# Optimization experiments

Hardware: AMD Instinct MI355X
Metric: run time of the kernel (lower is better)

The kernel has to match this reference:

```python
import jax, jax.numpy as jnp
import numpy as np

H, D, TOPK, NUM_B = 8, 64, 32, 1000
DIM, BATCH, SEQ = 1024, 4, 2048
SCALE = D ** -0.5


def _kaiming_like(key, shape, fan_in):
    # matches init.kaiming_uniform_(a=sqrt(5)) => U(-1/sqrt(fan_in), 1/sqrt(fan_in)) scale
    bound = 1.0 / np.sqrt(fan_in)
    return jax.random.uniform(key, shape, jnp.float32, -bound, bound)


def setup_inputs() -> dict:
    key = jax.random.key(0)
    ks = jax.random.split(key, 7)
    inner = H * D
    x = jax.random.normal(ks[0], (BATCH, SEQ, DIM), jnp.float32)
    W_qv = _kaiming_like(ks[1], (DIM, 2 * inner), DIM)
    W_out = _kaiming_like(ks[2], (inner, DIM), inner)
    b_out = jnp.zeros((DIM,), jnp.float32)
    b_mat = _kaiming_like(ks[3], (NUM_B, D, D), D)
    k_vec = _kaiming_like(ks[4], (NUM_B, D), D)
    o_vec = _kaiming_like(ks[5], (NUM_B, D), D)
    return {"x": x, "W_qv": W_qv, "W_out": W_out, "b_out": b_out,
            "b_mat": b_mat, "k_vec": k_vec, "o_vec": o_vec}


def reference(x, W_qv, W_out, b_out, b_mat, k_vec, o_vec):
    B, I, _ = x.shape
    qv = x @ W_qv                                   # (B, I, 2*H*D)
    q, v = jnp.split(qv, 2, axis=-1)

    def to_bh(t):                                    # 'b i (h d) -> (b h) i d'
        return t.reshape(B, I, H, D).transpose(0, 2, 1, 3).reshape(B * H, I, D)

    q, v = to_bh(q), to_bh(v)
    sim = jnp.einsum('nd,bid->bin', k_vec, q) * SCALE        # (B*H, I, num_b)
    t, b_inds = jax.lax.top_k(sim, TOPK)                     # (B*H, I, K) each
    attn = jax.nn.softmax(t, axis=-1)
    # torch einsum 'b i k d d, b i d -> b i k d' (repeated d) == diagonal of brains
    diag_b = jnp.diagonal(b_mat, axis1=-2, axis2=-1)         # (num_b, D)
    membr_pot = diag_b[b_inds] * v[:, :, None, :]            # (B*H, I, K, D)
    spike_proba = jax.nn.sigmoid(membr_pot)
    # straight-through rounding
    spike = spike_proba + jax.lax.stop_gradient(jnp.round(spike_proba) - spike_proba)
    nrt = spike * o_vec[b_inds]                              # (B*H, I, K, D)
    # psi starts as zeros_like(o) and is scatter-written at b_inds (last-write on dups)
    psi = jnp.zeros_like(o_vec).at[b_inds].set((1.0 - spike_proba) * membr_pot)
    out = jnp.einsum('bikd,bik->bid', nrt, attn)             # (B*H, I, D)
    out = out.reshape(B, H, I, D).transpose(0, 2, 1, 3).reshape(B, I, H * D)
    return out @ W_out + b_out, psi
```

## Files before the change

### kernel.cpp

```cpp
#include <hip/hip_runtime.h>
#include <math.h>

#define H_     8
#define D_     64
#define TOPK_  32
#define NUMB_  1000
#define DIM_   1024
#define BATCH_ 4
#define SEQ_   2048
#define INNER_ 512
#define TOK_   (BATCH_*SEQ_)
#define ROWS_  (BATCH_*H_*SEQ_)

#define PH_TOK_  4096
#define PH_ROWS_ 32768


__global__ void k0_prep(const float* __restrict__ b_mat,
                        const float* __restrict__ k_vec,
                        float* __restrict__ diagD,
                        float* __restrict__ kT,
                        int*   __restrict__ psiRow) {
    int t = blockIdx.x * 256 + threadIdx.x;
    if (t < NUMB_ * D_) {
        int n = t >> 6, d = t & 63;
        diagD[t] = b_mat[n * (D_ * D_) + d * (D_ + 1)];
        kT[d * NUMB_ + n] = k_vec[t];
    }
    if (t < NUMB_) psiRow[t] = -1;
}

#define BK1 16
__global__ __launch_bounds__(256) void k1_qv(const float* __restrict__ x,
                                             const float* __restrict__ Wqv,
                                             double* __restrict__ Qh,
                                             float*  __restrict__ V,
                                             int tokBase) {
    __shared__ float xs[64][BK1 + 1];
    __shared__ float ws[BK1][64 + 1];
    const int tx = threadIdx.x & 15, ty = threadIdx.x >> 4;
    const int mBase = tokBase + blockIdx.y * 64;
    const int nBase = blockIdx.x * 64;

    double acc[4][4];
#pragma unroll
    for (int a = 0; a < 4; a++)
#pragma unroll
        for (int b = 0; b < 4; b++) acc[a][b] = 0.0;

    for (int k0 = 0; k0 < DIM_; k0 += BK1) {
        for (int i = threadIdx.x; i < 64 * BK1; i += 256) {
            int r = i >> 4, kk = i & 15;
            xs[r][kk] = x[(size_t)(mBase + r) * DIM_ + k0 + kk];
        }
        for (int i = threadIdx.x; i < BK1 * 64; i += 256) {
            int kk = i >> 6, c = i & 63;
            ws[kk][c] = Wqv[(size_t)(k0 + kk) * (2 * INNER_) + nBase + c];
        }
        __syncthreads();
#pragma unroll
        for (int kk = 0; kk < BK1; ++kk) {
            float xa[4], wb[4];
#pragma unroll
            for (int a = 0; a < 4; a++) xa[a] = xs[ty * 4 + a][kk];
#pragma unroll
            for (int b = 0; b < 4; b++) wb[b] = ws[kk][tx * 4 + b];
#pragma unroll
            for (int a = 0; a < 4; a++)
#pragma unroll
                for (int b = 0; b < 4; b++)
                    acc[a][b] += (double)xa[a] * (double)wb[b];
        }
        __syncthreads();
    }

    const int mr = mBase + ty * 4, nc = nBase + tx * 4;
    if (nc < INNER_) {
#pragma unroll
        for (int a = 0; a < 4; a++)
#pragma unroll
            for (int b = 0; b < 4; b++)
                Qh[(size_t)(mr - tokBase + a) * INNER_ + nc + b] = acc[a][b];
    } else {
#pragma unroll
        for (int a = 0; a < 4; a++)
#pragma unroll
            for (int b = 0; b < 4; b++)
                V[(size_t)(mr + a) * INNER_ + (nc - INNER_) + b] = (float)acc[a][b];
    }
}

__global__ __launch_bounds__(256) void k2_sim(const double* __restrict__ Qh,
                                              const float*  __restrict__ V,
                                              const float*  __restrict__ kT,
                                              const float*  __restrict__ diagD,
                                              const float*  __restrict__ o_vec,
                                              float* __restrict__ OutMid,
                                              int*   __restrict__ psiRow,
                                              int sBase0, int tokOff) {
    __shared__ double qld[4][4][64];
    const int lane = threadIdx.x & 63;
    const int wid  = threadIdx.x >> 6;
    const int g    = blockIdx.x * 4 + wid;
    const int sBase = sBase0 + g * 4;

#pragma unroll
    for (int r = 0; r < 4; r++) {
        int s = sBase + r;
        int b = s >> 14, h = (s >> 11) & 7, i = s & 2047;
        int tok = b * SEQ_ + i;
        qld[wid][r][lane] = Qh[(size_t)(tok - tokOff) * INNER_ + h * D_ + lane];
    }
    __syncthreads();

    double acc[4][16];
#pragma unroll
    for (int r = 0; r < 4; r++)
#pragma unroll
        for (int nb = 0; nb < 16; nb++) acc[r][nb] = 0.0;

    for (int d = 0; d < 64; ++d) {
        double q0 = qld[wid][0][d];
        double q1 = qld[wid][1][d];
        double q2 = qld[wid][2][d];
        double q3 = qld[wid][3][d];
        const float* kp = kT + d * NUMB_;
#pragma unroll
        for (int nb = 0; nb < 16; ++nb) {
            int n = nb * 64 + lane;
            float kv = (n < NUMB_) ? kp[n] : 0.f;
            double kd = (double)kv;
            acc[0][nb] += q0 * kd;
            acc[1][nb] += q1 * kd;
            acc[2][nb] += q2 * kd;
            acc[3][nb] += q3 * kd;
        }
    }

#pragma unroll
    for (int r = 0; r < 4; r++) {
        int s = sBase + r;
        int b = s >> 14, h = (s >> 11) & 7, i = s & 2047;
        int tok = b * SEQ_ + i;
        float vlane = V[(size_t)tok * INNER_ + h * D_ + lane];

        unsigned key[16];
#pragma unroll
        for (int nb = 0; nb < 16; ++nb) {
            int n = nb * 64 + lane;
            float f = (float)acc[r][nb];
            unsigned u = __float_as_uint(f);
            unsigned kk = (u & 0x80000000u) ? ~u : (u | 0x80000000u);
            key[nb] = (n < NUMB_) ? kk : 0u;
        }

        unsigned tau = 0u;
        for (int bit = 31; bit >= 0; --bit) {
            unsigned cand = tau | (1u << bit);
            int c = 0;
#pragma unroll
            for (int nb = 0; nb < 16; ++nb)
                c += __popcll(__ballot(key[nb] >= cand));
            if (c >= TOPK_) tau = cand;
        }

        float esum = 0.f, outAcc = 0.f;
        int cgt = 0;

#pragma unroll
        for (int nb = 0; nb < 16; ++nb) {
            bool isgt = (key[nb] > tau);
            unsigned long long mm = __ballot(isgt);
            cgt += __popcll(mm);
            if (isgt) atomicMax(psiRow + nb * 64 + lane, s);
            while (mm) {
                int l = __ffsll((long long)mm) - 1; mm &= mm - 1;
                int n = nb * 64 + l;
                double v = __shfl(acc[r][nb], l);
                float ek = expf((float)v * 0.125f);
                esum += ek;
                float dg = diagD[n * 64 + lane];
                float mpot = dg * vlane;
                if (mpot > 0.f) outAcc += ek * o_vec[n * 64 + lane];
            }
        }

        int needed = TOPK_ - cgt;
        int ceq = 0;
#pragma unroll
        for (int nb = 0; nb < 16; ++nb)
            ceq += __popcll(__ballot(key[nb] == tau));

        if (ceq == needed) {
#pragma unroll
            for (int nb = 0; nb < 16; ++nb) {
                bool iseq = (key[nb] == tau);
                unsigned long long mm = __ballot(iseq);
                if (iseq) atomicMax(psiRow + nb * 64 + lane, s);
                while (mm) {
                    int l = __ffsll((long long)mm) - 1; mm &= mm - 1;
                    int n = nb * 64 + l;
                    double v = __shfl(acc[r][nb], l);
                    float ek = expf((float)v * 0.125f);
                    esum += ek;
                    float dg = diagD[n * 64 + lane];
                    float mpot = dg * vlane;
                    if (mpot > 0.f) outAcc += ek * o_vec[n * 64 + lane];
                }
            }
        } else {
            unsigned takenMask = 0u;
            for (int t = 0; t < needed; ++t) {
                double bv = -1e300; int bn = 0x7fffffff;
#pragma unroll
                for (int nb = 0; nb < 16; ++nb) {
                    int n = nb * 64 + lane;
                    bool candt = (key[nb] == tau) && !(takenMask & (1u << nb))
                                 && (n < NUMB_);
                    double v = acc[r][nb];
                    if (candt && (v > bv || (v == bv && n < bn))) { bv = v; bn = n; }
                }
                for (int off = 32; off; off >>= 1) {
                    double ov = __shfl_xor(bv, off);
                    int    on = __shfl_xor(bn, off);
                    if (ov > bv || (ov == bv && on < bn)) { bv = ov; bn = on; }
                }
                if ((bn & 63) == lane) takenMask |= 1u << (bn >> 6);
                float ek = expf((float)bv * 0.125f);
                esum += ek;
                float dg = diagD[bn * 64 + lane];
                float mpot = dg * vlane;
                if (mpot > 0.f) outAcc += ek * o_vec[bn * 64 + lane];
                if (lane == 0) atomicMax(psiRow + bn, s);
            }
        }

        OutMid[(size_t)tok * INNER_ + h * D_ + lane] = outAcc / esum;
    }
}

#define BK3 16
__global__ __launch_bounds__(256) void k3_out(const float* __restrict__ A,
                                              const float* __restrict__ Wout,
                                              const float* __restrict__ bout,
                                              float* __restrict__ out) {
    __shared__ float as[64][BK3 + 1];
    __shared__ float bs[BK3][64 + 1];
    const int tx = threadIdx.x & 15, ty = threadIdx.x >> 4;
    const int mBase = blockIdx.y * 64, nBase = blockIdx.x * 64;

    float acc[4][4];
#pragma unroll
    for (int a = 0; a < 4; a++)
#pragma unroll
        for (int b = 0; b < 4; b++) acc[a][b] = 0.f;

    for (int k0 = 0; k0 < INNER_; k0 += BK3) {
        for (int i = threadIdx.x; i < 64 * BK3; i += 256) {
            int r = i >> 4, kk = i & 15;
            as[r][kk] = A[(size_t)(mBase + r) * INNER_ + k0 + kk];
        }
        for (int i = threadIdx.x; i < BK3 * 64; i += 256) {
            int kk = i >> 6, c = i & 63;
            bs[kk][c] = Wout[(size_t)(k0 + kk) * DIM_ + nBase + c];
        }
        __syncthreads();
#pragma unroll
        for (int kk = 0; kk < BK3; ++kk) {
            float xa[4], wb[4];
#pragma unroll
            for (int a = 0; a < 4; a++) xa[a] = as[ty * 4 + a][kk];
#pragma unroll
            for (int b = 0; b < 4; b++) wb[b] = bs[kk][tx * 4 + b];
#pragma unroll
            for (int a = 0; a < 4; a++)
#pragma unroll
                for (int b = 0; b < 4; b++)
                    acc[a][b] += xa[a] * wb[b];
        }
        __syncthreads();
    }

    const int mr = mBase + ty * 4, nc = nBase + tx * 4;
#pragma unroll
    for (int a = 0; a < 4; a++)
#pragma unroll
        for (int b = 0; b < 4; b++)
            out[(size_t)(mr + a) * DIM_ + nc + b] = acc[a][b] + bout[nc + b];
}

__global__ void k4_psi(const int*   __restrict__ psiRow,
                       const float* __restrict__ V,
                       const float* __restrict__ diagD,
                       float* __restrict__ psiOut) {
    int t = blockIdx.x * 256 + threadIdx.x;
    if (t >= NUMB_ * D_) return;
    int n = t >> 6, d = t & 63;
    int s = psiRow[n];
    float val = 0.f;
    if (s >= 0) {
        int b = s >> 14, h = (s >> 11) & 7, i = s & 2047;
        int tok = b * SEQ_ + i;
        float v  = V[(size_t)tok * INNER_ + h * D_ + d];
        float m  = diagD[t] * v;
        float sg = 1.f / (1.f + expf(-m));
        val = (1.f - sg) * m;
    }
    psiOut[t] = val;
}

extern "C" void kernel_launch(void* const* d_in, const int* in_sizes, int n_in,
                              void* d_out, int out_size, void* d_ws, size_t ws_size,
                              hipStream_t stream) {
    const float* x    = (const float*)d_in[0];
    const float* Wqv  = (const float*)d_in[1];
    const float* Wout = (const float*)d_in[2];
    const float* bout = (const float*)d_in[3];
    const float* bmat = (const float*)d_in[4];
    const float* kvec = (const float*)d_in[5];
    const float* ovec = (const float*)d_in[6];
    float* out = (float*)d_out;

    char* ws = (char*)d_ws;
    float*  diagD  = (float*) (ws);
    float*  kT     = (float*) (ws + 256000);
    int*    psiRow = (int*)   (ws + 512000);
    float*  V      = (float*) (ws + (1u  << 20));
    float*  OutMid = (float*) (ws + (17u << 20));
    double* Qh     = (double*)(ws + (33u << 20));

    k0_prep<<<(NUMB_ * D_ + 255) / 256, 256, 0, stream>>>(bmat, kvec, diagD, kT, psiRow);

    for (int p = 0; p < 2; ++p) {
        k1_qv <<<dim3(16, PH_TOK_ / 64), 256, 0, stream>>>(x, Wqv, Qh, V, p * PH_TOK_);
        k2_sim<<<PH_ROWS_ / 16, 256, 0, stream>>>(Qh, V, kT, diagD, ovec, OutMid,
                                                  psiRow, p * PH_ROWS_, p * PH_TOK_);
    }

    k3_out<<<dim3(16, 128), 256, 0, stream>>>(OutMid, Wout, bout, out);
    k4_psi<<<(NUMB_ * D_ + 255) / 256, 256, 0, stream>>>(psiRow, V, diagD,
                                                         out + (size_t)TOK_ * DIM_);
}
```

Baseline: 1.975 ms.

## Restructure top-k sim kernel to cut register pressure and serialize selected gathers

The similarity matmul in k2_sim now runs in four column sub-groups of 4x4 double accumulators with sched barriers, keeping only 32-bit order keys per row instead of a 4x16 double accumulator array. This is meant to lower VGPR pressure and spilling. Values are recovered from the keys by an inverse mapping. In the common no-tie case the top-32 entries are compacted into a shared list, giving a wave-parallel exp/sum and a fixed 32-step gather loop instead of a data-dependent ballot loop. diag and o_vec are interleaved into float2 so each gather is one load. The tie path recomputes exact double similarities for tied entries, which costs extra work on rare rows. exp is now taken from float-rounded keys, which matches the earlier float cast.

After: 4.595 ms. +132.6%, slower.

```diff
diff --git a/kernel.cpp b/kernel.cpp
--- a/kernel.cpp
+++ b/kernel.cpp
@@ -18,13 +18,14 @@
 
 __global__ void k0_prep(const float* __restrict__ b_mat,
                         const float* __restrict__ k_vec,
-                        float* __restrict__ diagD,
-                        float* __restrict__ kT,
-                        int*   __restrict__ psiRow) {
+                        const float* __restrict__ o_vec,
+                        float2* __restrict__ dgo,
+                        float*  __restrict__ kT,
+                        int*    __restrict__ psiRow) {
     int t = blockIdx.x * 256 + threadIdx.x;
     if (t < NUMB_ * D_) {
         int n = t >> 6, d = t & 63;
-        diagD[t] = b_mat[n * (D_ * D_) + d * (D_ + 1)];
+        dgo[t] = make_float2(b_mat[n * (D_ * D_) + d * (D_ + 1)], o_vec[t]);
         kT[d * NUMB_ + n] = k_vec[t];
     }
     if (t < NUMB_) psiRow[t] = -1;
@@ -90,19 +91,26 @@
     }
 }
 
-__global__ __launch_bounds__(256) void k2_sim(const double* __restrict__ Qh,
-                                              const float*  __restrict__ V,
-                                              const float*  __restrict__ kT,
-                                              const float*  __restrict__ diagD,
-                                              const float*  __restrict__ o_vec,
-                                              float* __restrict__ OutMid,
-                                              int*   __restrict__ psiRow,
-                                              int sBase0, int tokOff) {
+__device__ __forceinline__ unsigned ordkey(float f) {
+    unsigned u = __float_as_uint(f);
+    return (u & 0x80000000u) ? ~u : (u | 0x80000000u);
+}
+__device__ __forceinline__ float ordinv(unsigned k) {
+    return __uint_as_float((k & 0x80000000u) ? (k & 0x7fffffffu) : ~k);
+}
+
+__global__ __launch_bounds__(256, 1) void k2_sim(const double* __restrict__ Qh,
+                                                 const float*  __restrict__ V,
+                                                 const float*  __restrict__ kT,
+                                                 const float2* __restrict__ dgo,
+                                                 float* __restrict__ OutMid,
+                                                 int*   __restrict__ psiRow,
+                                                 int sBase0, int tokOff) {
     __shared__ double qld[4][4][64];
+    __shared__ uint2  mlist[4][TOPK_];
     const int lane = threadIdx.x & 63;
     const int wid  = threadIdx.x >> 6;
-    const int g    = blockIdx.x * 4 + wid;
-    const int sBase = sBase0 + g * 4;
+    const int sBase = sBase0 + (blockIdx.x * 4 + wid) * 4;
 
 #pragma unroll
     for (int r = 0; r < 4; r++) {
@@ -113,46 +121,53 @@
     }
     __syncthreads();
 
-    double acc[4][16];
-#pragma unroll
-    for (int r = 0; r < 4; r++)
-#pragma unroll
-        for (int nb = 0; nb < 16; nb++) acc[r][nb] = 0.0;
-
-    for (int d = 0; d < 64; ++d) {
-        double q0 = qld[wid][0][d];
-        double q1 = qld[wid][1][d];
-        double q2 = qld[wid][2][d];
-        double q3 = qld[wid][3][d];
-        const float* kp = kT + d * NUMB_;
-#pragma unroll
-        for (int nb = 0; nb < 16; ++nb) {
-            int n = nb * 64 + lane;
-            float kv = (n < NUMB_) ? kp[n] : 0.f;
-            double kd = (double)kv;
-            acc[0][nb] += q0 * kd;
-            acc[1][nb] += q1 * kd;
-            acc[2][nb] += q2 * kd;
-            acc[3][nb] += q3 * kd;
-        }
-    }
-
-#pragma unroll
-    for (int r = 0; r < 4; r++) {
-        int s = sBase + r;
-        int b = s >> 14, h = (s >> 11) & 7, i = s & 2047;
-        int tok = b * SEQ_ + i;
-        float vlane = V[(size_t)tok * INNER_ + h * D_ + lane];
-
-        unsigned key[16];
-#pragma unroll
-        for (int nb = 0; nb < 16; ++nb) {
-            int n = nb * 64 + lane;
-            float f = (float)acc[r][nb];
-            unsigned u = __float_as_uint(f);
-            unsigned kk = (u & 0x80000000u) ? ~u : (u | 0x80000000u);
-            key[nb] = (n < NUMB_) ? kk : 0u;
-        }
+    unsigned key[4][16];
+
+#define DO_SG(SG)                                                             \
+    {                                                                         \
+        double acc[4][4];                                                     \
+        _Pragma("unroll")                                                     \
+        for (int r = 0; r < 4; r++)                                           \
+            _Pragma("unroll")                                                 \
+            for (int j = 0; j < 4; j++) acc[r][j] = 0.0;                      \
+        for (int d = 0; d < 64; ++d) {                                        \
+            double q0 = qld[wid][0][d], q1 = qld[wid][1][d];                  \
+            double q2 = qld[wid][2][d], q3 = qld[wid][3][d];                  \
+            const float* kp = kT + d * NUMB_;                                 \
+            _Pragma("unroll")                                                 \
+            for (int j = 0; j < 4; j++) {                                     \
+                int n = ((SG) * 4 + j) * 64 + lane;                           \
+                float kv = (n < NUMB_) ? kp[n] : 0.f;                         \
+                double kd = (double)kv;                                       \
+                acc[0][j] += q0 * kd;                                         \
+                acc[1][j] += q1 * kd;                                         \
+                acc[2][j] += q2 * kd;                                         \
+                acc[3][j] += q3 * kd;                                         \
+            }                                                                 \
+        }                                                                     \
+        _Pragma("unroll")                                                     \
+        for (int r = 0; r < 4; r++)                                           \
+            _Pragma("unroll")                                                 \
+            for (int j = 0; j < 4; j++) {                                     \
+                int n = ((SG) * 4 + j) * 64 + lane;                           \
+                key[r][(SG) * 4 + j] =                                        \
+                    (n < NUMB_) ? ordkey((float)acc[r][j]) : 0u;              \
+            }                                                                 \
+    }                                                                         \
+    __builtin_amdgcn_sched_barrier(0);
+
+    DO_SG(0)
+    DO_SG(1)
+    DO_SG(2)
+    DO_SG(3)
+#undef DO_SG
+
+#pragma unroll 1
+    for (int r = 0; r < 4; ++r) {
+        const int s = sBase + r;
+        const int b = s >> 14, h = (s >> 11) & 7, ii = s & 2047;
+        const int tok = b * SEQ_ + ii;
+        const float vlane = V[(size_t)tok * INNER_ + h * D_ + lane];
 
         unsigned tau = 0u;
         for (int bit = 31; bit >= 0; --bit) {
@@ -160,64 +175,90 @@
             int c = 0;
 #pragma unroll
             for (int nb = 0; nb < 16; ++nb)
-                c += __popcll(__ballot(key[nb] >= cand));
+                c += __popcll(__ballot(key[r][nb] >= cand));
             if (c >= TOPK_) tau = cand;
         }
 
-        float esum = 0.f, outAcc = 0.f;
-        int cgt = 0;
-
+        int cgt = 0, ceq = 0;
 #pragma unroll
         for (int nb = 0; nb < 16; ++nb) {
-            bool isgt = (key[nb] > tau);
-            unsigned long long mm = __ballot(isgt);
-            cgt += __popcll(mm);
-            if (isgt) atomicMax(psiRow + nb * 64 + lane, s);
-            while (mm) {
-                int l = __ffsll((long long)mm) - 1; mm &= mm - 1;
-                int n = nb * 64 + l;
-                double v = __shfl(acc[r][nb], l);
-                float ek = expf((float)v * 0.125f);
-                esum += ek;
-                float dg = diagD[n * 64 + lane];
-                float mpot = dg * vlane;
-                if (mpot > 0.f) outAcc += ek * o_vec[n * 64 + lane];
-            }
-        }
-
-        int needed = TOPK_ - cgt;
-        int ceq = 0;
-#pragma unroll
-        for (int nb = 0; nb < 16; ++nb)
-            ceq += __popcll(__ballot(key[nb] == tau));
+            cgt += __popcll(__ballot(key[r][nb] > tau));
+            ceq += __popcll(__ballot(key[r][nb] == tau));
+        }
+        const int needed = TOPK_ - cgt;
+
+        float esum, outAcc = 0.f;
 
         if (ceq == needed) {
+            int base = 0;
 #pragma unroll
             for (int nb = 0; nb < 16; ++nb) {
-                bool iseq = (key[nb] == tau);
-                unsigned long long mm = __ballot(iseq);
-                if (iseq) atomicMax(psiRow + nb * 64 + lane, s);
+                unsigned kk = key[r][nb];
+                bool sel = (kk >= tau);
+                unsigned long long mm = __ballot(sel);
+                if (sel) {
+                    int n = nb * 64 + lane;
+                    int pos = base + __popcll(mm & ((1ull << lane) - 1ull));
+                    mlist[wid][pos] =
+                        make_uint2((unsigned)n, __float_as_uint(ordinv(kk)));
+                    atomicMax(psiRow + n, s);
+                }
+                base += __popcll(mm);
+            }
+            uint2 rec = mlist[wid][lane & 31];
+            float myek = expf(__uint_as_float(rec.y) * 0.125f);
+            float e = myek;
+#pragma unroll
+            for (int off = 1; off <= 16; off <<= 1)
+                e += __shfl_xor(e, off);
+            esum = e;
+#pragma unroll
+            for (int k = 0; k < TOPK_; ++k) {
+                int   nk = __shfl((int)rec.x, k);
+                float ek = __shfl(myek, k);
+                float2 g = dgo[nk * 64 + lane];
+                float mpot = g.x * vlane;
+                if (mpot > 0.f) outAcc += ek * g.y;
+            }
+        } else {
+            esum = 0.f;
+#pragma unroll
+            for (int nb = 0; nb < 16; ++nb) {
+                unsigned kk = key[r][nb];
+                bool isgt = (kk > tau);
+                unsigned long long mm = __ballot(isgt);
+                if (isgt) atomicMax(psiRow + nb * 64 + lane, s);
                 while (mm) {
-                    int l = __ffsll((long long)mm) - 1; mm &= mm - 1;
+                    int l = __ffsll((unsigned long long)mm) - 1; mm &= mm - 1;
                     int n = nb * 64 + l;
-                    double v = __shfl(acc[r][nb], l);
-                    float ek = expf((float)v * 0.125f);
+                    unsigned kr = (unsigned)__shfl((int)kk, l);
+                    float ek = expf(ordinv(kr) * 0.125f);
                     esum += ek;
-                    float dg = diagD[n * 64 + lane];
-                    float mpot = dg * vlane;
-                    if (mpot > 0.f) outAcc += ek * o_vec[n * 64 + lane];
-                }
-            }
-        } else {
+                    float2 g = dgo[n * 64 + lane];
+                    float mpot = g.x * vlane;
+                    if (mpot > 0.f) outAcc += ek * g.y;
+                }
+            }
+            double eqsim[16];
+#pragma unroll
+            for (int nb = 0; nb < 16; ++nb) {
+                eqsim[nb] = -1e300;
+                if (key[r][nb] == tau) {
+                    double sacc = 0.0;
+                    for (int d = 0; d < 64; ++d)
+                        sacc += qld[wid][r][d] *
+                                (double)kT[d * NUMB_ + nb * 64 + lane];
+                    eqsim[nb] = sacc;
+                }
+            }
             unsigned takenMask = 0u;
             for (int t = 0; t < needed; ++t) {
                 double bv = -1e300; int bn = 0x7fffffff;
 #pragma unroll
                 for (int nb = 0; nb < 16; ++nb) {
+                    bool candt = (key[r][nb] == tau) && !(takenMask & (1u << nb));
+                    double v = eqsim[nb];
                     int n = nb * 64 + lane;
-                    bool candt = (key[nb] == tau) && !(takenMask & (1u << nb))
-                                 && (n < NUMB_);
-                    double v = acc[r][nb];
                     if (candt && (v > bv || (v == bv && n < bn))) { bv = v; bn = n; }
                 }
                 for (int off = 32; off; off >>= 1) {
@@ -228,9 +269,9 @@
                 if ((bn & 63) == lane) takenMask |= 1u << (bn >> 6);
                 float ek = expf((float)bv * 0.125f);
                 esum += ek;
-                float dg = diagD[bn * 64 + lane];
-                float mpot = dg * vlane;
-                if (mpot > 0.f) outAcc += ek * o_vec[bn * 64 + lane];
+                float2 g = dgo[bn * 64 + lane];
+                float mpot = g.x * vlane;
+                if (mpot > 0.f) outAcc += ek * g.y;
                 if (lane == 0) atomicMax(psiRow + bn, s);
             }
         }
@@ -289,9 +330,9 @@
             out[(size_t)(mr + a) * DIM_ + nc + b] = acc[a][b] + bout[nc + b];
 }
 
-__global__ void k4_psi(const int*   __restrict__ psiRow,
-                       const float* __restrict__ V,
-                       const float* __restrict__ diagD,
+__global__ void k4_psi(const int*    __restrict__ psiRow,
+                       const float*  __restrict__ V,
+                       const float2* __restrict__ dgo,
                        float* __restrict__ psiOut) {
     int t = blockIdx.x * 256 + threadIdx.x;
     if (t >= NUMB_ * D_) return;
@@ -302,7 +343,7 @@
         int b = s >> 14, h = (s >> 11) & 7, i = s & 2047;
         int tok = b * SEQ_ + i;
         float v  = V[(size_t)tok * INNER_ + h * D_ + d];
-        float m  = diagD[t] * v;
+        float m  = dgo[t].x * v;
         float sg = 1.f / (1.f + expf(-m));
         val = (1.f - sg) * m;
     }
@@ -322,22 +363,23 @@
     float* out = (float*)d_out;
 
     char* ws = (char*)d_ws;
-    float*  diagD  = (float*) (ws);
-    float*  kT     = (float*) (ws + 256000);
-    int*    psiRow = (int*)   (ws + 512000);
+    float2* dgo    = (float2*)(ws);
+    float*  kT     = (float*) (ws + 512000);
+    int*    psiRow = (int*)   (ws + 768000);
     float*  V      = (float*) (ws + (1u  << 20));
     float*  OutMid = (float*) (ws + (17u << 20));
     double* Qh     = (double*)(ws + (33u << 20));
 
-    k0_prep<<<(NUMB_ * D_ + 255) / 256, 256, 0, stream>>>(bmat, kvec, diagD, kT, psiRow);
+    k0_prep<<<(NUMB_ * D_ + 255) / 256, 256, 0, stream>>>(bmat, kvec, ovec,
+                                                          dgo, kT, psiRow);
 
     for (int p = 0; p < 2; ++p) {
         k1_qv <<<dim3(16, PH_TOK_ / 64), 256, 0, stream>>>(x, Wqv, Qh, V, p * PH_TOK_);
-        k2_sim<<<PH_ROWS_ / 16, 256, 0, stream>>>(Qh, V, kT, diagD, ovec, OutMid,
+        k2_sim<<<PH_ROWS_ / 16, 256, 0, stream>>>(Qh, V, kT, dgo, OutMid,
                                                   psiRow, p * PH_ROWS_, p * PH_TOK_);
     }
 
     k3_out<<<dim3(16, 128), 256, 0, stream>>>(OutMid, Wout, bout, out);
-    k4_psi<<<(NUMB_ * D_ + 255) / 256, 256, 0, stream>>>(psiRow, V, diagD,
+    k4_psi<<<(NUMB_ * D_ + 255) / 256, 256, 0, stream>>>(psiRow, V, dgo,
                                                          out + (size_t)TOK_ * DIM_);
 }
```
